# Kernel tuning notes

Measured on AMD Instinct MI355X. Metric: run time of the kernel, lower is better.

## Reference

```python
import jax, jax.numpy as jnp
import numpy as np

B, T, D, H = 1, 4096, 1024, 16
HD = D // H  # 64
ROPE_BASE = 10000.0


def rotate_half(x):
    x1, x2 = jnp.split(x, 2, axis=-1)
    return jnp.concatenate([-x2, x1], axis=-1)


def rope_sin_cos(t, head_dim, dtype):
    inv_freq = 1.0 / (ROPE_BASE ** (jnp.arange(0, head_dim, 2, dtype=jnp.float32) / head_dim))
    pos = jnp.arange(t, dtype=jnp.float32)
    freqs = pos[:, None] * inv_freq[None, :]          # [T, HD/2]
    emb = jnp.concatenate([freqs, freqs], axis=-1)    # [T, HD]
    return jnp.sin(emb).astype(dtype), jnp.cos(emb).astype(dtype)


def setup_inputs() -> dict:
    key = jax.random.key(0)
    kx, kq, kp = jax.random.split(key, 3)
    scale = 0.02
    x = jax.random.normal(kx, (B, T, D), dtype=jnp.float32)
    W_qkv = jax.random.normal(kq, (3 * D, D), dtype=jnp.float32) * scale  # torch Linear weight [out,in]
    W_proj = jax.random.normal(kp, (D, D), dtype=jnp.float32) * scale
    return {"x": x, "W_qkv": W_qkv, "W_proj": W_proj}


def reference(x, W_qkv, W_proj):
    b, t, d = x.shape
    qkv = jnp.einsum('btd,ed->bte', x, W_qkv)                 # [B,T,3D]
    qkv = qkv.reshape(b, t, 3, H, HD)
    q, k, v = (qkv[:, :, i].transpose(0, 2, 1, 3) for i in range(3))  # each [B,H,T,HD]
    sin, cos = rope_sin_cos(t, HD, x.dtype)                    # [T,HD]
    q = q * cos + rotate_half(q) * sin
    k = k * cos + rotate_half(k) * sin
    scores = jnp.einsum('bhqd,bhkd->bhqk', q, k) / jnp.sqrt(jnp.asarray(HD, x.dtype))
    mask = jnp.triu(jnp.full((t, t), -jnp.inf, dtype=x.dtype), k=1)
    attn = jax.nn.softmax(scores + mask, axis=-1)
    out = jnp.einsum('bhqk,bhkd->bhqd', attn, v)               # [B,H,T,HD]
    out = out.transpose(0, 2, 1, 3).reshape(b, t, d)
    return jnp.einsum('btd,ed->bte', out, W_proj)
```

## Files before the change

### kernel.cpp

```cpp
#include <hip/hip_runtime.h>
#include <hip/hip_bf16.h>
#include <stdint.h>

#define TSEQ 4096
#define DM   1024
#define NH   16
#define HD   64
#define NQKV 3072

typedef unsigned short u16;
typedef unsigned int   u32;
typedef __attribute__((ext_vector_type(8)))  short bf16x8;
typedef __attribute__((ext_vector_type(4)))  float f32x4;
typedef __attribute__((ext_vector_type(16))) float f32x16;
typedef __attribute__((ext_vector_type(4)))  int   i32x4;

static __device__ __forceinline__ u16 f2bf(float f) {
  u32 u = __float_as_uint(f);
  u32 r = (u + 0x7FFFu + ((u >> 16) & 1u)) >> 16;
  return (u16)r;
}
static __device__ __forceinline__ float bf2f(u16 u) {
  return __uint_as_float(((u32)u) << 16);
}
static __device__ __forceinline__ u32 cvt_pk_bf16(float lo, float hi) {
  u32 r;
  asm("v_cvt_pk_bf16_f32 %0, %1, %2" : "=v"(r) : "v"(lo), "v"(hi));
  return r;
}
static __device__ __forceinline__ float fexp2(float x) {
  float r;
  asm("v_exp_f32 %0, %1" : "=v"(r) : "v"(x));
  return r;
}

#define GLL16(g, l) __builtin_amdgcn_global_load_lds( \
    (const __attribute__((address_space(1))) u32*)(g), \
    (__attribute__((address_space(3))) u32*)(l), 16, 0, 0)

#define N4X  (TSEQ * DM / 4)
#define N4Q  (NQKV * DM / 4)
#define N4P  (DM * DM / 4)
__global__ void cast3_kernel(const float* __restrict__ x, u16* __restrict__ xo,
                             const float* __restrict__ wq, u16* __restrict__ wqo,
                             const float* __restrict__ wp, u16* __restrict__ wpo) {
  int i = blockIdx.x * 256 + threadIdx.x;
  const float* in; u16* out; int k;
  if (i < N4X)            { in = x;  out = xo;  k = i; }
  else if (i < N4X + N4Q) { in = wq; out = wqo; k = i - N4X; }
  else if (i < N4X + N4Q + N4P) { in = wp; out = wpo; k = i - N4X - N4Q; }
  else return;
  float4 v = ((const float4*)in)[k];
  ushort4 o;
  o.x = f2bf(v.x); o.y = f2bf(v.y); o.z = f2bf(v.z); o.w = f2bf(v.w);
  ((ushort4*)out)[k] = o;
}

__global__ void rope_table(float* __restrict__ sT, float* __restrict__ cT) {
  int i = blockIdx.x * 256 + threadIdx.x;
  int t = i >> 5, j = i & 31;
  float inv = exp2f((float)j * (-13.287712379549449f / 32.0f));
  float ang = (float)t * inv;
  sT[i] = sinf(ang);
  cT[i] = cosf(ang);
}

__global__ __launch_bounds__(256) void gemm_qkv(const u16* __restrict__ A,
                                                const u16* __restrict__ B,
                                                const float* __restrict__ sT,
                                                const float* __restrict__ cT,
                                                u16* __restrict__ Qo,
                                                u16* __restrict__ Ko,
                                                u16* __restrict__ Vo)
{
  const int K = DM;
  __shared__ __align__(16) u16 As[2][64 * 32];
  __shared__ __align__(16) u16 Bs[2][128 * 32];
  const int tid  = threadIdx.x;
  const int wave = tid >> 6, lane = tid & 63;
  const int l15  = lane & 15, lh = lane >> 4;
  const int wr   = wave >> 1, wc = wave & 1;

  const int nwg = gridDim.x * gridDim.y;
  int lin = blockIdx.y * gridDim.x + blockIdx.x;
  lin = (lin & 7) * (nwg >> 3) + (lin >> 3);
  const size_t bm = (size_t)(lin / gridDim.x);
  const size_t bn = (size_t)(lin % gridDim.x);

  f32x4 acc[2][4] = {};

  const u16* Ab = A + bm * 64 * (size_t)K;
  const u16* Bb = B + bn * 128 * (size_t)K;

  const int ea  = wave * 512 + lane * 8,       ra  = ea  >> 5, ca  = ea  & 31;
  const int eb1 = (4 + wave) * 512 + lane * 8, rb1 = eb1 >> 5, cb1 = eb1 & 31;

  GLL16(Ab + (size_t)ra * K + ca,   &As[0][wave * 512]);
  GLL16(Bb + (size_t)ra * K + ca,   &Bs[0][wave * 512]);
  GLL16(Bb + (size_t)rb1 * K + cb1, &Bs[0][(4 + wave) * 512]);
  asm volatile("s_waitcnt vmcnt(0)" ::: "memory");
  __syncthreads();

  int cur = 0;
  for (int k0 = 0; k0 < K; k0 += 32, cur ^= 1) {
    if (k0 + 32 < K) {
      const int kn = k0 + 32;
      GLL16(Ab + (size_t)ra * K + kn + ca,   &As[cur ^ 1][wave * 512]);
      GLL16(Bb + (size_t)ra * K + kn + ca,   &Bs[cur ^ 1][wave * 512]);
      GLL16(Bb + (size_t)rb1 * K + kn + cb1, &Bs[cur ^ 1][(4 + wave) * 512]);
    }

    bf16x8 af[2], bfr[4];
#pragma unroll
    for (int m = 0; m < 2; ++m)
      af[m] = *(const bf16x8*)(&As[cur][(wr * 32 + m * 16 + l15) * 32 + lh * 8]);
#pragma unroll
    for (int n = 0; n < 4; ++n)
      bfr[n] = *(const bf16x8*)(&Bs[cur][(wc * 64 + n * 16 + l15) * 32 + lh * 8]);
    __builtin_amdgcn_s_setprio(1);
#pragma unroll
    for (int m = 0; m < 2; ++m)
#pragma unroll
      for (int n = 0; n < 4; ++n)
        acc[m][n] = __builtin_amdgcn_mfma_f32_16x16x32_bf16(af[m], bfr[n], acc[m][n], 0, 0, 0);
    __builtin_amdgcn_s_setprio(0);

    asm volatile("s_waitcnt vmcnt(0)" ::: "memory");
    __syncthreads();
  }

  const float QSC = 0.125f * 1.4426950408889634f;
  const int gcb = (int)(bn * 128) + wc * 64;
  const int rg  = gcb >> 10;
  const int hh2 = (gcb >> 6) & 15;
  const size_t hb = (size_t)hh2 * 128;

  if (rg < 2) {
    u16* dst = rg ? Ko : Qo;
    const float sc = rg ? 1.f : QSC;
#pragma unroll
    for (int m = 0; m < 2; ++m)
#pragma unroll
      for (int r = 0; r < 4; ++r) {
        int t = (int)(bm * 64) + wr * 32 + m * 16 + lh * 4 + r;
        size_t tb = (hb + (t >> 5)) * 2048 + (size_t)(t & 31) * 8;
#pragma unroll
        for (int n = 0; n < 2; ++n) {
          int d  = n * 16 + l15;
          int d2 = d + 32;
          float s = sT[t * 32 + d], c = cT[t * 32 + d];
          float v1 = acc[m][n][r], v2 = acc[m][n + 2][r];
          dst[tb + (d  >> 4) * 512 + ((d  >> 3) & 1) * 256 + (d  & 7)] =
              f2bf((v1 * c - v2 * s) * sc);
          dst[tb + (d2 >> 4) * 512 + ((d2 >> 3) & 1) * 256 + (d2 & 7)] =
              f2bf((v2 * c + v1 * s) * sc);
        }
      }
  } else {
#pragma unroll
    for (int m = 0; m < 2; ++m)
#pragma unroll
      for (int r = 0; r < 4; ++r) {
        int t = (int)(bm * 64) + wr * 32 + m * 16 + lh * 4 + r;
        size_t tb = (hb + (t >> 5)) * 2048 + (size_t)((t >> 4) & 1) * 512 +
                    ((t >> 3) & 1) * 256 + (t & 7);
#pragma unroll
        for (int n = 0; n < 4; ++n) {
          int d = n * 16 + l15;
          Vo[tb + (size_t)(d >> 5) * 1024 + (size_t)(d & 31) * 8] = f2bf(acc[m][n][r]);
        }
      }
  }
}

__global__ __launch_bounds__(256) void gemm_proj(const u16* __restrict__ A,
                                                 const u16* __restrict__ B,
                                                 float* __restrict__ Cout,
                                                 int M, int N, int K)
{
  __shared__ __align__(16) u16 As[2][64 * 32];
  __shared__ __align__(16) u16 Bs[2][64 * 32];
  const int tid  = threadIdx.x;
  const int wave = tid >> 6, lane = tid & 63;
  const int l15  = lane & 15, lh = lane >> 4;
  const int wr   = wave >> 1, wc = wave & 1;

  const int nwg = gridDim.x * gridDim.y;
  int lin = blockIdx.y * gridDim.x + blockIdx.x;
  lin = (lin & 7) * (nwg >> 3) + (lin >> 3);
  const size_t bm = (size_t)(lin / gridDim.x);
  const size_t bn = (size_t)(lin % gridDim.x);

  f32x4 acc[2][2] = {};

  const u16* Ab = A + bm * 64 * (size_t)K;
  const u16* Bb = B + bn * 64 * (size_t)K;

  const int ea = wave * 512 + lane * 8, ra = ea >> 5, ca = ea & 31;

  GLL16(Ab + (size_t)ra * K + ca, &As[0][wave * 512]);
  GLL16(Bb + (size_t)ra * K + ca, &Bs[0][wave * 512]);
  asm volatile("s_waitcnt vmcnt(0)" ::: "memory");
  __syncthreads();

  int cur = 0;
  for (int k0 = 0; k0 < K; k0 += 32, cur ^= 1) {
    if (k0 + 32 < K) {
      const int kn = k0 + 32;
      GLL16(Ab + (size_t)ra * K + kn + ca, &As[cur ^ 1][wave * 512]);
      GLL16(Bb + (size_t)ra * K + kn + ca, &Bs[cur ^ 1][wave * 512]);
    }

    bf16x8 af[2], bfr[2];
#pragma unroll
    for (int m = 0; m < 2; ++m)
      af[m] = *(const bf16x8*)(&As[cur][(wr * 32 + m * 16 + l15) * 32 + lh * 8]);
#pragma unroll
    for (int n = 0; n < 2; ++n)
      bfr[n] = *(const bf16x8*)(&Bs[cur][(wc * 32 + n * 16 + l15) * 32 + lh * 8]);
    __builtin_amdgcn_s_setprio(1);
#pragma unroll
    for (int m = 0; m < 2; ++m)
#pragma unroll
      for (int n = 0; n < 2; ++n)
        acc[m][n] = __builtin_amdgcn_mfma_f32_16x16x32_bf16(af[m], bfr[n], acc[m][n], 0, 0, 0);
    __builtin_amdgcn_s_setprio(0);

    asm volatile("s_waitcnt vmcnt(0)" ::: "memory");
    __syncthreads();
  }

#pragma unroll
  for (int m = 0; m < 2; ++m)
#pragma unroll
    for (int n = 0; n < 2; ++n)
#pragma unroll
      for (int r = 0; r < 4; ++r) {
        size_t row = bm * 64 + wr * 32 + m * 16 + lh * 4 + r;
        size_t col = bn * 64 + wc * 32 + n * 16 + l15;
        Cout[row * N + col] = acc[m][n][r];
      }
}

__global__ __launch_bounds__(256, 4) void fattn(const u16* __restrict__ Qf,
                                                const u16* __restrict__ Kf,
                                                const u16* __restrict__ Vf,
                                                u16* __restrict__ Op0,
                                                u16* __restrict__ Op123,
                                                float2* __restrict__ lmb)
{
  __shared__ __align__(16) u16 smem[8192];

  const int bid = blockIdx.x;
  const int h   = bid & (NH - 1);
  const int g   = (bid >> 4) & 3;
  const int pr  = bid >> 6;
  const int tid = threadIdx.x;
  const int wave = tid >> 6, lane = tid & 63;
  const int l31 = lane & 31, hh = lane >> 5;
  const int lb  = lane * 8;

  const size_t hbase = (size_t)h * (TSEQ * HD);
  const u16* kg = Kf + hbase;
  const u16* vg = Vf + hbase;
  u16* const Og = g ? (Op123 + (size_t)(g - 1) * (TSEQ * DM)) : Op0;

  for (int ph = 0; ph < 2; ++ph) {
    const int qt  = ph ? (31 - pr) : pr;
    const int q0  = qt * 128;
    const int per = qt + 1;
    const int kt0 = g * per, kt1 = kt0 + per;
    const int qw0 = q0 + wave * 32;
    const int qgl = qw0 + l31;

    f32x16 oacc0 = {}, oacc1 = {};
    float mrun = 0.f, lrunp = 0.f;

    bf16x8 qf[4];
    {
      const u16* qp = Qf + hbase + (size_t)(qt * 4 + wave) * 2048;
#pragma unroll
      for (int kc = 0; kc < 4; ++kc)
        qf[kc] = *(const bf16x8*)(qp + kc * 512 + lb);
    }

    GLL16(kg + (size_t)kt0 * 2048 + tid * 8, smem + tid * 8);
    GLL16(vg + (size_t)kt0 * 2048 + tid * 8, smem + 4096 + tid * 8);
    asm volatile("s_waitcnt vmcnt(0)" ::: "memory");
    __syncthreads();

    for (int kt = kt0; kt < kt1; ++kt) {
      const int cur = (kt - kt0) & 1;
      if (kt + 1 < kt1) {
        GLL16(kg + (size_t)(kt + 1) * 2048 + tid * 8, smem + (cur ^ 1) * 2048 + tid * 8);
        GLL16(vg + (size_t)(kt + 1) * 2048 + tid * 8, smem + 4096 + (cur ^ 1) * 2048 + tid * 8);
      }
      const u16* kb = smem + cur * 2048;
      const u16* vb = smem + 4096 + cur * 2048;
      const int kv0 = kt * 32;

      const float mz = (kt == kt0) ? 0.f : -mrun;
      f32x16 s0;
      __builtin_amdgcn_s_setprio(1);
      {
        f32x16 z;
#pragma unroll
        for (int i2 = 0; i2 < 16; ++i2) z[i2] = mz;
        bf16x8 kf0 = *(const bf16x8*)(kb + lb);
        s0 = __builtin_amdgcn_mfma_f32_32x32x16_bf16(kf0, qf[0], z, 0, 0, 0);
      }
#pragma unroll
      for (int kc = 1; kc < 4; ++kc) {
        bf16x8 kf = *(const bf16x8*)(kb + kc * 512 + lb);
        s0 = __builtin_amdgcn_mfma_f32_32x32x16_bf16(kf, qf[kc], s0, 0, 0, 0);
      }
      __builtin_amdgcn_s_setprio(0);

      if (kv0 + 31 > qw0) {
#pragma unroll
        for (int r = 0; r < 16; ++r) {
          int kvr = kv0 + (r & 3) + 8 * (r >> 2) + 4 * hh;
          if (kvr > qgl) s0[r] = -3.0e38f;
        }
      }

      if (kt == kt0) {
        float tm = -3.0e38f;
#pragma unroll
        for (int r = 0; r < 16; ++r) tm = fmaxf(tm, s0[r]);
        tm = fmaxf(tm, __shfl_xor(tm, 32));
        mrun = tm;
#pragma unroll
        for (int r = 0; r < 16; ++r) s0[r] -= mrun;
      }

      float rs = 0.f;
#pragma unroll
      for (int r = 0; r < 16; ++r) {
        s0[r] = fexp2(s0[r]);
        rs += s0[r];
      }
      lrunp += rs;

      bf16x8 pf[2];
#pragma unroll
      for (int kc = 0; kc < 2; ++kc) {
        const int e = 8 * kc;
        u32 Xa = cvt_pk_bf16(s0[e + 0], s0[e + 1]);
        u32 Xb = cvt_pk_bf16(s0[e + 2], s0[e + 3]);
        u32 Ya = cvt_pk_bf16(s0[e + 4], s0[e + 5]);
        u32 Yb = cvt_pk_bf16(s0[e + 6], s0[e + 7]);
        asm volatile("v_permlane32_swap_b32 %0, %1" : "+v"(Xa), "+v"(Ya));
        asm volatile("v_permlane32_swap_b32 %0, %1" : "+v"(Xb), "+v"(Yb));
        union { u32 u[4]; bf16x8 v; } pu;
        pu.u[0] = Xa; pu.u[1] = Xb; pu.u[2] = Ya; pu.u[3] = Yb;
        pf[kc] = pu.v;
      }

      __builtin_amdgcn_s_setprio(1);
#pragma unroll
      for (int s2 = 0; s2 < 2; ++s2) {
        bf16x8 v0 = *(const bf16x8*)(vb + (0 * 2 + s2) * 512 + lb);
        bf16x8 v1 = *(const bf16x8*)(vb + (1 * 2 + s2) * 512 + lb);
        oacc0 = __builtin_amdgcn_mfma_f32_32x32x16_bf16(v0, pf[s2], oacc0, 0, 0, 0);
        oacc1 = __builtin_amdgcn_mfma_f32_32x32x16_bf16(v1, pf[s2], oacc1, 0, 0, 0);
      }
      __builtin_amdgcn_s_setprio(0);

      asm volatile("s_waitcnt vmcnt(0)" ::: "memory");
      __syncthreads();
    }

    {
      float lr = lrunp + __shfl_xor(lrunp, 32);
      float inv = 1.f / lr;
      u16* scr = smem + wave * 2048;
#pragma unroll
      for (int dt = 0; dt < 2; ++dt)
#pragma unroll
        for (int rq = 0; rq < 4; ++rq) {
          float v0 = (dt ? oacc1[4 * rq + 0] : oacc0[4 * rq + 0]) * inv;
          float v1 = (dt ? oacc1[4 * rq + 1] : oacc0[4 * rq + 1]) * inv;
          float v2 = (dt ? oacc1[4 * rq + 2] : oacc0[4 * rq + 2]) * inv;
          float v3 = (dt ? oacc1[4 * rq + 3] : oacc0[4 * rq + 3]) * inv;
          uint2 wv;
          wv.x = cvt_pk_bf16(v0, v1);
          wv.y = cvt_pk_bf16(v2, v3);
          int g2 = 4 * dt + rq;
          *(uint2*)(scr + l31 * 64 + ((g2 ^ (l31 & 7)) * 8) + 4 * hh) = wv;
        }
      asm volatile("s_waitcnt lgkmcnt(0)" ::: "memory");
      __builtin_amdgcn_sched_barrier(0);
      const int q  = lane >> 1;
      const int dh = lane & 1;
#pragma unroll
      for (int c2 = 0; c2 < 4; ++c2) {
        int gg = dh * 4 + c2;
        i32x4 v = *(const i32x4*)(scr + q * 64 + ((gg ^ (q & 7)) * 8));
        *(i32x4*)(Og + (size_t)(qw0 + q) * DM + h * HD + dh * 32 + c2 * 8) = v;
      }
      if (hh == 0)
        lmb[((size_t)g * NH + h) * TSEQ + qgl] = make_float2(mrun, lr);
    }
    __syncthreads();
  }
}

__global__ void merge_o(const u16* __restrict__ Op0, const u16* __restrict__ Op123,
                        const float2* __restrict__ lmb, u16* __restrict__ Ob) {
  int i = blockIdx.x * 256 + threadIdx.x;
  int q  = i >> 7;
  int c8 = (i & 127) * 8;
  int h  = c8 >> 6;
  float2 s0 = lmb[(size_t)h * TSEQ + q];
  float2 s1 = lmb[((size_t)NH + h) * TSEQ + q];
  float2 s2 = lmb[((size_t)2 * NH + h) * TSEQ + q];
  float2 s3 = lmb[((size_t)3 * NH + h) * TSEQ + q];
  float m  = fmaxf(fmaxf(s0.x, s1.x), fmaxf(s2.x, s3.x));
  float w0 = fexp2(s0.x - m) * s0.y;
  float w1 = fexp2(s1.x - m) * s1.y;
  float w2 = fexp2(s2.x - m) * s2.y;
  float w3 = fexp2(s3.x - m) * s3.y;
  float inv = 1.f / (w0 + w1 + w2 + w3);
  float a0 = w0 * inv, a1 = w1 * inv, a2 = w2 * inv, a3 = w3 * inv;
  size_t off = (size_t)q * DM + c8;
  i32x4 u0 = *(const i32x4*)(Op0 + off);
  i32x4 u1 = *(const i32x4*)(Op123 + off);
  i32x4 u2 = *(const i32x4*)(Op123 + (size_t)(TSEQ * DM) + off);
  i32x4 u3 = *(const i32x4*)(Op123 + 2 * (size_t)(TSEQ * DM) + off);
  const u16* p0 = (const u16*)&u0;
  const u16* p1 = (const u16*)&u1;
  const u16* p2 = (const u16*)&u2;
  const u16* p3 = (const u16*)&u3;
  union { u16 o[8]; i32x4 v; } r;
#pragma unroll
  for (int e = 0; e < 8; ++e)
    r.o[e] = f2bf(a0 * bf2f(p0[e]) + a1 * bf2f(p1[e]) +
                  a2 * bf2f(p2[e]) + a3 * bf2f(p3[e]));
  *(i32x4*)(Ob + off) = r.v;
}

extern "C" void kernel_launch(void* const* d_in, const int* in_sizes, int n_in,
                              void* d_out, int out_size, void* d_ws, size_t ws_size,
                              hipStream_t stream)
{
  const float* x     = (const float*)d_in[0];
  const float* wqkv  = (const float*)d_in[1];
  const float* wproj = (const float*)d_in[2];
  float* out = (float*)d_out;

  char* ws = (char*)d_ws;
  size_t off = 0;
  u16* xb   = (u16*)(ws + off); off += (size_t)TSEQ * DM * 2;
  u16* wqb  = (u16*)(ws + off); off += (size_t)NQKV * DM * 2;
  u16* wpb  = (u16*)(ws + off); off += (size_t)DM * DM * 2;
  u16* qkvb = (u16*)(ws + off); off += (size_t)TSEQ * NQKV * 2;
  u16* Qb   = (u16*)(ws + off); off += (size_t)NH * TSEQ * HD * 2;
  u16* Kb   = (u16*)(ws + off); off += (size_t)NH * TSEQ * HD * 2;
  u16* Vb   = (u16*)(ws + off); off += (size_t)NH * TSEQ * HD * 2;
  u16* Ob   = (u16*)(ws + off); off += (size_t)TSEQ * DM * 2;
  float* sT = (float*)(ws + off); off += (size_t)TSEQ * 32 * 4;
  float* cT = (float*)(ws + off); off += (size_t)TSEQ * 32 * 4;

  u16*    Op123 = qkvb;
  float2* lmb   = (float2*)wqb;

  const int ncast = N4X + N4Q + N4P;
  cast3_kernel<<<(ncast + 255) / 256, 256, 0, stream>>>(x, xb, wqkv, wqb, wproj, wpb);
  rope_table<<<(TSEQ * 32) / 256, 256, 0, stream>>>(sT, cT);

  gemm_qkv<<<dim3(NQKV / 128, TSEQ / 64), 256, 0, stream>>>(xb, wqb, sT, cT, Qb, Kb, Vb);

  fattn<<<NH * 64, 256, 0, stream>>>(Qb, Kb, Vb, Ob, Op123, lmb);

  merge_o<<<(TSEQ * DM / 8) / 256, 256, 0, stream>>>(Ob, Op123, lmb, Ob);

  gemm_proj<<<dim3(DM / 64, TSEQ / 64), 256, 0, stream>>>(Ob, wpb, out, TSEQ, DM, DM);
}
```

Baseline: 135.1 us.

## Load GEMM operands directly from global into registers, dropping LDS staging

```diff
diff --git a/kernel.cpp b/kernel.cpp
--- a/kernel.cpp
+++ b/kernel.cpp
@@ -74,8 +74,6 @@
                                                 u16* __restrict__ Vo)
 {
   const int K = DM;
-  __shared__ __align__(16) u16 As[2][64 * 32];
-  __shared__ __align__(16) u16 Bs[2][128 * 32];
   const int tid  = threadIdx.x;
   const int wave = tid >> 6, lane = tid & 63;
   const int l15  = lane & 15, lh = lane >> 4;
@@ -89,44 +87,41 @@
 
   f32x4 acc[2][4] = {};
 
-  const u16* Ab = A + bm * 64 * (size_t)K;
-  const u16* Bb = B + bn * 128 * (size_t)K;
-
-  const int ea  = wave * 512 + lane * 8,       ra  = ea  >> 5, ca  = ea  & 31;
-  const int eb1 = (4 + wave) * 512 + lane * 8, rb1 = eb1 >> 5, cb1 = eb1 & 31;
-
-  GLL16(Ab + (size_t)ra * K + ca,   &As[0][wave * 512]);
-  GLL16(Bb + (size_t)ra * K + ca,   &Bs[0][wave * 512]);
-  GLL16(Bb + (size_t)rb1 * K + cb1, &Bs[0][(4 + wave) * 512]);
-  asm volatile("s_waitcnt vmcnt(0)" ::: "memory");
-  __syncthreads();
-
-  int cur = 0;
-  for (int k0 = 0; k0 < K; k0 += 32, cur ^= 1) {
-    if (k0 + 32 < K) {
-      const int kn = k0 + 32;
-      GLL16(Ab + (size_t)ra * K + kn + ca,   &As[cur ^ 1][wave * 512]);
-      GLL16(Bb + (size_t)ra * K + kn + ca,   &Bs[cur ^ 1][wave * 512]);
-      GLL16(Bb + (size_t)rb1 * K + kn + cb1, &Bs[cur ^ 1][(4 + wave) * 512]);
+  const u16* Ap = A + ((size_t)(bm * 64 + wr * 32 + l15)) * K + lh * 8;
+  const u16* Bp = B + ((size_t)(bn * 128 + wc * 64 + l15)) * K + lh * 8;
+
+  bf16x8 aA[2], bA[4], aB[2], bB[4];
+#pragma unroll
+  for (int m = 0; m < 2; ++m) aA[m] = *(const bf16x8*)(Ap + (size_t)m * 16 * K);
+#pragma unroll
+  for (int n = 0; n < 4; ++n) bA[n] = *(const bf16x8*)(Bp + (size_t)n * 16 * K);
+
+  for (int k0 = 0; k0 < K; k0 += 64) {
+#pragma unroll
+    for (int m = 0; m < 2; ++m) aB[m] = *(const bf16x8*)(Ap + (size_t)m * 16 * K + k0 + 32);
+#pragma unroll
+    for (int n = 0; n < 4; ++n) bB[n] = *(const bf16x8*)(Bp + (size_t)n * 16 * K + k0 + 32);
+    __builtin_amdgcn_s_setprio(1);
+#pragma unroll
+    for (int m = 0; m < 2; ++m)
+#pragma unroll
+      for (int n = 0; n < 4; ++n)
+        acc[m][n] = __builtin_amdgcn_mfma_f32_16x16x32_bf16(aA[m], bA[n], acc[m][n], 0, 0, 0);
+    __builtin_amdgcn_s_setprio(0);
+
+    if (k0 + 64 < K) {
+#pragma unroll
+      for (int m = 0; m < 2; ++m) aA[m] = *(const bf16x8*)(Ap + (size_t)m * 16 * K + k0 + 64);
+#pragma unroll
+      for (int n = 0; n < 4; ++n) bA[n] = *(const bf16x8*)(Bp + (size_t)n * 16 * K + k0 + 64);
     }
-
-    bf16x8 af[2], bfr[4];
-#pragma unroll
-    for (int m = 0; m < 2; ++m)
-      af[m] = *(const bf16x8*)(&As[cur][(wr * 32 + m * 16 + l15) * 32 + lh * 8]);
-#pragma unroll
-    for (int n = 0; n < 4; ++n)
-      bfr[n] = *(const bf16x8*)(&Bs[cur][(wc * 64 + n * 16 + l15) * 32 + lh * 8]);
     __builtin_amdgcn_s_setprio(1);
 #pragma unroll
     for (int m = 0; m < 2; ++m)
 #pragma unroll
       for (int n = 0; n < 4; ++n)
-        acc[m][n] = __builtin_amdgcn_mfma_f32_16x16x32_bf16(af[m], bfr[n], acc[m][n], 0, 0, 0);
+        acc[m][n] = __builtin_amdgcn_mfma_f32_16x16x32_bf16(aB[m], bB[n], acc[m][n], 0, 0, 0);
     __builtin_amdgcn_s_setprio(0);
-
-    asm volatile("s_waitcnt vmcnt(0)" ::: "memory");
-    __syncthreads();
   }
 
   const float QSC = 0.125f * 1.4426950408889634f;
@@ -178,8 +173,6 @@
                                                  float* __restrict__ Cout,
                                                  int M, int N, int K)
 {
-  __shared__ __align__(16) u16 As[2][64 * 32];
-  __shared__ __align__(16) u16 Bs[2][64 * 32];
   const int tid  = threadIdx.x;
   const int wave = tid >> 6, lane = tid & 63;
   const int l15  = lane & 15, lh = lane >> 4;
@@ -193,41 +186,41 @@
 
   f32x4 acc[2][2] = {};
 
-  const u16* Ab = A + bm * 64 * (size_t)K;
-  const u16* Bb = B + bn * 64 * (size_t)K;
-
-  const int ea = wave * 512 + lane * 8, ra = ea >> 5, ca = ea & 31;
-
-  GLL16(Ab + (size_t)ra * K + ca, &As[0][wave * 512]);
-  GLL16(Bb + (size_t)ra * K + ca, &Bs[0][wave * 512]);
-  asm volatile("s_waitcnt vmcnt(0)" ::: "memory");
-  __syncthreads();
-
-  int cur = 0;
-  for (int k0 = 0; k0 < K; k0 += 32, cur ^= 1) {
-    if (k0 + 32 < K) {
-      const int kn = k0 + 32;
-      GLL16(Ab + (size_t)ra * K + kn + ca, &As[cur ^ 1][wave * 512]);
-      GLL16(Bb + (size_t)ra * K + kn + ca, &Bs[cur ^ 1][wave * 512]);
+  const u16* Ap = A + ((size_t)(bm * 64 + wr * 32 + l15)) * K + lh * 8;
+  const u16* Bp = B + ((size_t)(bn * 64 + wc * 32 + l15)) * K + lh * 8;
+
+  bf16x8 aA[2], bA[2], aB[2], bB[2];
+#pragma unroll
+  for (int m = 0; m < 2; ++m) aA[m] = *(const bf16x8*)(Ap + (size_t)m * 16 * K);
+#pragma unroll
+  for (int n = 0; n < 2; ++n) bA[n] = *(const bf16x8*)(Bp + (size_t)n * 16 * K);
+
+  for (int k0 = 0; k0 < K; k0 += 64) {
+#pragma unroll
+    for (int m = 0; m < 2; ++m) aB[m] = *(const bf16x8*)(Ap + (size_t)m * 16 * K + k0 + 32);
+#pragma unroll
+    for (int n = 0; n < 2; ++n) bB[n] = *(const bf16x8*)(Bp + (size_t)n * 16 * K + k0 + 32);
+    __builtin_amdgcn_s_setprio(1);
+#pragma unroll
+    for (int m = 0; m < 2; ++m)
+#pragma unroll
+      for (int n = 0; n < 2; ++n)
+        acc[m][n] = __builtin_amdgcn_mfma_f32_16x16x32_bf16(aA[m], bA[n], acc[m][n], 0, 0, 0);
+    __builtin_amdgcn_s_setprio(0);
+
+    if (k0 + 64 < K) {
+#pragma unroll
+      for (int m = 0; m < 2; ++m) aA[m] = *(const bf16x8*)(Ap + (size_t)m * 16 * K + k0 + 64);
+#pragma unroll
+      for (int n = 0; n < 2; ++n) bA[n] = *(const bf16x8*)(Bp + (size_t)n * 16 * K + k0 + 64);
     }
-
-    bf16x8 af[2], bfr[2];
-#pragma unroll
-    for (int m = 0; m < 2; ++m)
-      af[m] = *(const bf16x8*)(&As[cur][(wr * 32 + m * 16 + l15) * 32 + lh * 8]);
-#pragma unroll
-    for (int n = 0; n < 2; ++n)
-      bfr[n] = *(const bf16x8*)(&Bs[cur][(wc * 32 + n * 16 + l15) * 32 + lh * 8]);
     __builtin_amdgcn_s_setprio(1);
 #pragma unroll
     for (int m = 0; m < 2; ++m)
 #pragma unroll
       for (int n = 0; n < 2; ++n)
-        acc[m][n] = __builtin_amdgcn_mfma_f32_16x16x32_bf16(af[m], bfr[n], acc[m][n], 0, 0, 0);
+        acc[m][n] = __builtin_amdgcn_mfma_f32_16x16x32_bf16(aB[m], bB[n], acc[m][n], 0, 0, 0);
     __builtin_amdgcn_s_setprio(0);
-
-    asm volatile("s_waitcnt vmcnt(0)" ::: "memory");
-    __syncthreads();
   }
 
 #pragma unroll
```

New measurement: 257.4 us. 1.91x slower.
